# Kernel tuning notes

Hardware: AMD Instinct MI355X
Metric: run time of the kernel (lower is better)

Reference implementation:

```python
import jax, jax.numpy as jnp
import numpy as np

D = 256
H = 4
HD = D // H


def rotate_half(x):
    xp = x.reshape(x.shape[:-1] + (-1, 2))
    x1, x2 = xp[..., 0], xp[..., 1]
    return jnp.stack((-x2, x1), axis=-1).reshape(x.shape)


def apply_rope(freqs, t):
    # freqs: [2, B, 1, N, HD]; t: [B, H, N, HD]
    return t * freqs[0] + rotate_half(t) * freqs[1]


def layernorm(x, g, b, eps=1e-5):
    m = jnp.mean(x, axis=-1, keepdims=True)
    v = jnp.var(x, axis=-1, keepdims=True)
    return (x - m) * jax.lax.rsqrt(v + eps) * g + b


def ffn(z, W1, b1, g, be, W2, b2):
    h = layernorm(z @ W1 + b1, g, be)
    h = jax.nn.gelu(h, approximate=False)
    return h @ W2 + b2


def heads_split(t):
    B, N, _ = t.shape
    return t.reshape(B, N, H, HD).transpose(0, 2, 1, 3)  # [B,H,N,HD]


def heads_merge(t):
    B, h, N, hd = t.shape
    return t.transpose(0, 2, 1, 3).reshape(B, N, h * hd)


def sdpa(q, k, v):
    s = q.shape[-1] ** (-0.5)
    sim = jnp.einsum('bhid,bhjd->bhij', q, k) * s
    attn = jax.nn.softmax(sim, axis=-1)
    return jnp.einsum('bhij,bhjd->bhid', attn, v)


def self_block(x, enc, Wqkv, bqkv, Wo, bo, W1, b1, g, be, W2, b2):
    B, N, _ = x.shape
    qkv = (x @ Wqkv + bqkv).reshape(B, N, H, HD, 3).transpose(0, 2, 1, 3, 4)
    q, k, v = qkv[..., 0], qkv[..., 1], qkv[..., 2]
    q = apply_rope(enc, q)
    k = apply_rope(enc, k)
    msg = heads_merge(sdpa(q, k, v)) @ Wo + bo
    return x + ffn(jnp.concatenate([x, msg], axis=-1), W1, b1, g, be, W2, b2)


def cross_block(x0, x1, Wqk, bqk, Wv, bv, Wo, bo, W1, b1, g, be, W2, b2):
    qk0 = heads_split(x0 @ Wqk + bqk)
    qk1 = heads_split(x1 @ Wqk + bqk)
    v0 = heads_split(x0 @ Wv + bv)
    v1 = heads_split(x1 @ Wv + bv)
    s = HD ** (-0.5)
    qk0 = qk0 * (s ** 0.5)
    qk1 = qk1 * (s ** 0.5)
    sim = jnp.einsum('bhid,bhjd->bhij', qk0, qk1)
    attn01 = jax.nn.softmax(sim, axis=-1)
    attn10 = jax.nn.softmax(sim.transpose(0, 1, 3, 2), axis=-1)
    m0 = jnp.einsum('bhij,bhjd->bhid', attn01, v1)
    m1 = jnp.einsum('bhij,bhjd->bhid', attn10, v0)
    m0 = heads_merge(m0) @ Wo + bo
    m1 = heads_merge(m1) @ Wo + bo
    x0 = x0 + ffn(jnp.concatenate([x0, m0], axis=-1), W1, b1, g, be, W2, b2)
    x1 = x1 + ffn(jnp.concatenate([x1, m1], axis=-1), W1, b1, g, be, W2, b2)
    return x0, x1


def setup_inputs() -> dict:
    key = jax.random.key(0)
    ks = jax.random.split(key, 24)
    B, N = 4, 2048
    desc0 = jax.random.normal(ks[0], (B, N, D), jnp.float32)
    desc1 = jax.random.normal(ks[1], (B, N, D), jnp.float32)
    encoding0 = jax.random.uniform(ks[2], (2, B, 1, N, HD), jnp.float32)
    encoding1 = jax.random.uniform(ks[3], (2, B, 1, N, HD), jnp.float32)

    def lin(k, fin, fout):
        k1, k2 = jax.random.split(k)
        W = jax.random.normal(k1, (fin, fout), jnp.float32) * (fin ** -0.5)
        b = jax.random.normal(k2, (fout,), jnp.float32) * 0.01
        return W, b

    Wqkv, bqkv = lin(ks[4], D, 3 * D)
    Wo_s, bo_s = lin(ks[5], D, D)
    W1_s, b1_s = lin(ks[6], 2 * D, 2 * D)
    g_s = jnp.ones((2 * D,), jnp.float32)
    be_s = jnp.zeros((2 * D,), jnp.float32)
    W2_s, b2_s = lin(ks[7], 2 * D, D)
    Wqk_c, bqk_c = lin(ks[8], D, D)
    Wv_c, bv_c = lin(ks[9], D, D)
    Wo_c, bo_c = lin(ks[10], D, D)
    W1_c, b1_c = lin(ks[11], 2 * D, 2 * D)
    g_c = jnp.ones((2 * D,), jnp.float32)
    be_c = jnp.zeros((2 * D,), jnp.float32)
    W2_c, b2_c = lin(ks[12], 2 * D, D)
    return dict(desc0=desc0, desc1=desc1, encoding0=encoding0, encoding1=encoding1,
                Wqkv=Wqkv, bqkv=bqkv, Wo_s=Wo_s, bo_s=bo_s,
                W1_s=W1_s, b1_s=b1_s, g_s=g_s, be_s=be_s, W2_s=W2_s, b2_s=b2_s,
                Wqk_c=Wqk_c, bqk_c=bqk_c, Wv_c=Wv_c, bv_c=bv_c, Wo_c=Wo_c, bo_c=bo_c,
                W1_c=W1_c, b1_c=b1_c, g_c=g_c, be_c=be_c, W2_c=W2_c, b2_c=b2_c)


def reference(desc0, desc1, encoding0, encoding1,
              Wqkv, bqkv, Wo_s, bo_s, W1_s, b1_s, g_s, be_s, W2_s, b2_s,
              Wqk_c, bqk_c, Wv_c, bv_c, Wo_c, bo_c, W1_c, b1_c, g_c, be_c, W2_c, b2_c):
    d0 = self_block(desc0, encoding0, Wqkv, bqkv, Wo_s, bo_s, W1_s, b1_s, g_s, be_s, W2_s, b2_s)
    d1 = self_block(desc1, encoding1, Wqkv, bqkv, Wo_s, bo_s, W1_s, b1_s, g_s, be_s, W2_s, b2_s)
    return cross_block(d0, d1, Wqk_c, bqk_c, Wv_c, bv_c, Wo_c, bo_c, W1_c, b1_c, g_c, be_c, W2_c, b2_c)
```

## Files before the change

kernel.cpp:

```cpp
#include <hip/hip_runtime.h>
#include <math.h>

#define BB 4
#define HH 4
#define NN 2048
#define DD 256
#define HDIM 64
#define NTOK 8192
#define NTOK2 16384

typedef __attribute__((ext_vector_type(8))) __bf16 bf16x8;
typedef __attribute__((ext_vector_type(8))) unsigned short ushort8;
typedef __attribute__((ext_vector_type(4))) float floatx4;
typedef __attribute__((ext_vector_type(4))) short short4v;

union U8 { ushort8 u; bf16x8 b; };
union U4 { unsigned int u[2]; unsigned long long l; short4v s; };

#define MFMA16(a, b, c) __builtin_amdgcn_mfma_f32_16x16x16bf16_1k(a, b, c, 0, 0, 0)

__device__ __forceinline__ unsigned short f2bf(float x) {
    unsigned int u = __float_as_uint(x);
    u += 0x7FFF + ((u >> 16) & 1);
    return (unsigned short)(u >> 16);
}
__device__ __forceinline__ float bf2f(unsigned short u) {
    return __uint_as_float(((unsigned int)u) << 16);
}
__device__ __forceinline__ unsigned int cvtpk(float a, float b) {
    unsigned int r;
    asm("v_cvt_pk_bf16_f32 %0, %1, %2" : "=v"(r) : "v"(a), "v"(b));
    return r;
}
__device__ __forceinline__ floatx4 fmax4(floatx4 a, floatx4 b) {
    floatx4 r;
    r[0] = fmaxf(a[0], b[0]); r[1] = fmaxf(a[1], b[1]);
    r[2] = fmaxf(a[2], b[2]); r[3] = fmaxf(a[3], b[3]);
    return r;
}

struct WTab {
    const float* w[7];
    unsigned short* o[7];
    int K[7];
    int N[7];
    int st[7];
    int t0[8];
};

__global__ __launch_bounds__(256) void wtrans(WTab tab)
{
    __shared__ float lds[32][33];
    const int t = threadIdx.x;
    int bid = blockIdx.x;
    int s = 0;
    while (bid >= tab.t0[s + 1]) s++;
    const int ti = bid - tab.t0[s];
    const int K = tab.K[s], N = tab.N[s], st = tab.st[s];
    const int tx = ti % (N / 32), ty = ti / (N / 32);
    const int k0 = ty * 32, n0 = tx * 32;
    const float* W = tab.w[s];
    unsigned short* Wt = tab.o[s];

    {
        int r = t >> 3, c = (t & 7) * 4;
        float4 a = *(const float4*)&W[(size_t)(k0 + r) * N + n0 + c];
        lds[r][c] = a.x; lds[r][c+1] = a.y; lds[r][c+2] = a.z; lds[r][c+3] = a.w;
    }
    __syncthreads();
    {
        int n = t >> 3, kq = (t & 7) * 4;
        ushort4 p;
        p.x = f2bf(lds[kq+0][n]); p.y = f2bf(lds[kq+1][n]);
        p.z = f2bf(lds[kq+2][n]); p.w = f2bf(lds[kq+3][n]);
        *(ushort4*)&Wt[(size_t)(n0 + n) * st + k0 + kq] = p;
    }
}

__global__ __launch_bounds__(256) void wfuse(
    const float* __restrict__ Wo_s, const float* __restrict__ W1_s,
    unsigned short* __restrict__ o_s,
    const float* __restrict__ Wo_c, const float* __restrict__ W1_c,
    unsigned short* __restrict__ o_c)
{
    __shared__ float wo[32][33];
    __shared__ float w1[32][68];
    const int t = threadIdx.x;
    const int bid = blockIdx.x;
    const int seg = bid >> 6, ti_ = bid & 63;
    const int i0 = (ti_ >> 3) * 32, n0 = (ti_ & 7) * 64;
    const float* Wo  = seg ? Wo_c : Wo_s;
    const float* W1b = (seg ? W1_c : W1_s) + 256 * 512;
    unsigned short* out = seg ? o_c : o_s;
    const int ti = t >> 3, tn = t & 7;

    float acc[8] = {};
    for (int jc = 0; jc < 256; jc += 32) {
        {
            int r = t >> 3, c = (t & 7) * 4;
            *(float4*)&wo[r][c] = *(const float4*)&Wo[(size_t)(i0 + r) * 256 + jc + c];
            int c8 = (t & 7) * 8;
            *(float4*)&w1[r][c8]     = *(const float4*)&W1b[(size_t)(jc + r) * 512 + n0 + c8];
            *(float4*)&w1[r][c8 + 4] = *(const float4*)&W1b[(size_t)(jc + r) * 512 + n0 + c8 + 4];
        }
        __syncthreads();
        #pragma unroll
        for (int j = 0; j < 32; j++) {
            float a = wo[ti][j];
            #pragma unroll
            for (int e = 0; e < 8; e++) acc[e] += a * w1[j][tn * 8 + e];
        }
        __syncthreads();
    }
    #pragma unroll
    for (int e = 0; e < 8; e++)
        out[(size_t)(n0 + tn * 8 + e) * 512 + 256 + i0 + ti] = f2bf(acc[e]);
}

__global__ __launch_bounds__(256) void bfuse(
    const float* bo_s, const float* W1_s, const float* b1_s, float* bs,
    const float* bo_c, const float* W1_c, const float* b1_c, float* bc)
{
    __shared__ float r[4];
    const int bid = blockIdx.x;
    const int seg = bid >> 9, n = bid & 511;
    const float* bo  = seg ? bo_c : bo_s;
    const float* W1b = (seg ? W1_c : W1_s) + 256 * 512;
    const float* b1  = seg ? b1_c : b1_s;
    float* out       = seg ? bc : bs;
    const int j = threadIdx.x;
    float a = bo[j] * W1b[(size_t)j * 512 + n];
    #pragma unroll
    for (int o = 32; o > 0; o >>= 1) a += __shfl_xor(a, o, 64);
    if ((j & 63) == 0) r[j >> 6] = a;
    __syncthreads();
    if (j == 0) out[n] = b1[n] + r[0] + r[1] + r[2] + r[3];
}

__global__ __launch_bounds__(256) void gemm_mfma(
    const unsigned short* __restrict__ A, int lda,
    const unsigned short* __restrict__ Wt, int K,
    const float* __restrict__ bias, const float* __restrict__ bias2, int mode,
    float* outF, unsigned short* outH0, unsigned short* outH1,
    unsigned short* outH2,
    int ldc, const float* R0, const float* R1)
{
    __shared__ __align__(16) unsigned short As[64 * 72];
    __shared__ __align__(16) unsigned short Bs[128 * 72];
    const int t = threadIdx.x;
    const int w = t >> 6, lane = t & 63, quad = lane >> 4, l15 = lane & 15;
    const int m0 = blockIdx.y * 64, n0 = blockIdx.x * 128;
    const int wn = w * 32;
    const int sar = t >> 2, sac = (t & 3) * 16;
    const int sbr = t >> 1, sbc = (t & 1) * 32;

    const unsigned short* Ap = A  + (size_t)(m0 + sar) * lda + sac;
    const unsigned short* Bp = Wt + (size_t)(n0 + sbr) * K   + sbc;

    ushort8 pa0 = *(const ushort8*)(Ap);
    ushort8 pa1 = *(const ushort8*)(Ap + 8);
    ushort8 pb0 = *(const ushort8*)(Bp);
    ushort8 pb1 = *(const ushort8*)(Bp + 8);
    ushort8 pb2 = *(const ushort8*)(Bp + 16);
    ushort8 pb3 = *(const ushort8*)(Bp + 24);

    floatx4 acc[4][2];
    #pragma unroll
    for (int i = 0; i < 4; i++)
        #pragma unroll
        for (int j = 0; j < 2; j++) acc[i][j] = (floatx4){0.f, 0.f, 0.f, 0.f};

    const int nk = K >> 6;
    for (int kk = 0; kk < nk; kk++) {
        *(ushort8*)&As[sar * 72 + sac]      = pa0;
        *(ushort8*)&As[sar * 72 + sac + 8]  = pa1;
        *(ushort8*)&Bs[sbr * 72 + sbc]      = pb0;
        *(ushort8*)&Bs[sbr * 72 + sbc + 8]  = pb1;
        *(ushort8*)&Bs[sbr * 72 + sbc + 16] = pb2;
        *(ushort8*)&Bs[sbr * 72 + sbc + 24] = pb3;
        __syncthreads();
        if (kk + 1 < nk) {
            int ko = (kk + 1) * 64;
            pa0 = *(const ushort8*)(Ap + ko);
            pa1 = *(const ushort8*)(Ap + ko + 8);
            pb0 = *(const ushort8*)(Bp + ko);
            pb1 = *(const ushort8*)(Bp + ko + 8);
            pb2 = *(const ushort8*)(Bp + ko + 16);
            pb3 = *(const ushort8*)(Bp + ko + 24);
        }
        #pragma unroll
        for (int kh = 0; kh < 2; kh++) {
            U8 af[4], bf[2];
            #pragma unroll
            for (int i = 0; i < 4; i++)
                af[i].u = *(const ushort8*)&As[(i * 16 + l15) * 72 + kh * 32 + quad * 8];
            #pragma unroll
            for (int j = 0; j < 2; j++)
                bf[j].u = *(const ushort8*)&Bs[(wn + j * 16 + l15) * 72 + kh * 32 + quad * 8];
            #pragma unroll
            for (int i = 0; i < 4; i++)
                #pragma unroll
                for (int j = 0; j < 2; j++)
                    acc[i][j] = __builtin_amdgcn_mfma_f32_16x16x32_bf16(af[i].b, bf[j].b, acc[i][j], 0, 0, 0);
        }
        __syncthreads();
    }

    #pragma unroll
    for (int i = 0; i < 4; i++) {
        #pragma unroll
        for (int j = 0; j < 2; j++) {
            int col = n0 + wn + j * 16 + l15;
            float bv = (mode == 2 && col >= 256) ? bias2[col & 255] : bias[col];
            #pragma unroll
            for (int r = 0; r < 4; r++) {
                int grow = m0 + i * 16 + quad * 4 + r;
                float v = acc[i][j][r] + bv;
                if (mode == 1) {
                    outH0[(size_t)grow * ldc + col] = f2bf(v);
                } else if (mode == 2) {
                    int cc = col & 255;
                    int h = cc >> 6, d = cc & 63;
                    int ds = grow >> 13, b = (grow >> 11) & 3, n = grow & 2047;
                    int bh = ds * 16 + b * 4 + h;
                    if (col < 256)
                        outH0[((size_t)bh * NN + n) * HDIM + d] = f2bf(v);
                    else
                        outH1[((size_t)bh * HDIM + d) * NN + n] = f2bf(v);
                } else if (mode == 3) {
                    int sel = col % 3, cc = col / 3;
                    int h = cc >> 6, d = cc & 63;
                    int ds = grow >> 13, b = (grow >> 11) & 3, n = grow & 2047;
                    int bh = ds * 16 + b * 4 + h;
                    if (sel == 0)
                        outH0[((size_t)bh * NN + n) * HDIM + d] = f2bf(v);
                    else if (sel == 1)
                        outH1[((size_t)bh * NN + n) * HDIM + d] = f2bf(v);
                    else
                        outH2[((size_t)bh * HDIM + d) * NN + n] = f2bf(v);
                } else {
                    const float* R = (grow < NTOK) ? R0 : R1;
                    float vv = v + R[(size_t)(grow & 8191) * 256 + col];
                    outF[(size_t)grow * 256 + col] = vv;
                    if (outH0) outH0[(size_t)grow * 256 + col] = f2bf(vv);
                    if (outH1) outH1[(size_t)grow * 512 + col] = f2bf(vv);
                }
            }
        }
    }
}

__global__ __launch_bounds__(256) void rope_k(unsigned short* __restrict__ qb,
                                              unsigned short* __restrict__ kb,
                                              const float* __restrict__ enc0,
                                              const float* __restrict__ enc1)
{
    int i = blockIdx.x * 256 + threadIdx.x;
    int dp = (i & 31) * 2;
    int n  = (i >> 5) & (NN - 1);
    int h  = (i >> 16) & 3;
    int b  = (i >> 18) & 3;
    int ds = (i >> 20) & 1;
    int bf = (i >> 21) & 1;
    unsigned short* tq = (bf ? kb : qb) +
        (((size_t)(ds * 16 + b * 4 + h)) * NN + n) * HDIM + dp;
    const float* e0 = (ds ? enc1 : enc0) + ((size_t)b * NN + n) * HDIM + dp;
    const float* e1 = e0 + (size_t)BB * NN * HDIM;
    float x0 = bf2f(tq[0]), x1 = bf2f(tq[1]);
    float y0 = x0 * e0[0] - x1 * e1[0];
    float y1 = x1 * e0[1] + x0 * e1[1];
    tq[0] = f2bf(y0); tq[1] = f2bf(y1);
}

__global__ __launch_bounds__(256) void flash_attn(
    const unsigned short* __restrict__ Q, const unsigned short* __restrict__ K,
    const unsigned short* __restrict__ V, unsigned short* __restrict__ O,
    int ldo, int kvx, float qscale)
{
    __shared__ __align__(16) unsigned short Ks[2][64 * 72];
    __shared__ __align__(16) unsigned short Vt[2][64 * 72];

    const int t    = threadIdx.x;
    const int w    = t >> 6;
    const int lane = t & 63;
    const int quad = lane >> 4;
    const int l15  = lane & 15;
    const int bh   = blockIdx.y;
    const int kbh  = bh ^ kvx;
    const int q0   = blockIdx.x * 64;

    const unsigned short* Qb  = Q + (size_t)bh  * NN * HDIM;
    const unsigned short* Kb  = K + (size_t)kbh * NN * HDIM;
    const unsigned short* VTb = V + (size_t)kbh * NN * HDIM;

    const int srf = t >> 3, scf = (t & 7) * 8;

    bf16x8 qf0, qf1;
    {
        const int qrow = q0 + w * 16 + l15;
        U8 r0, r1, x0, x1;
        r0.u = *(const ushort8*)&Qb[(size_t)qrow * HDIM + quad * 8];
        r1.u = *(const ushort8*)&Qb[(size_t)qrow * HDIM + 32 + quad * 8];
        #pragma unroll
        for (int j = 0; j < 8; j++) {
            x0.u[j] = f2bf(bf2f(r0.u[j]) * qscale);
            x1.u[j] = f2bf(bf2f(r1.u[j]) * qscale);
        }
        qf0 = x0.b; qf1 = x1.b;
    }

    floatx4 o[4];
    #pragma unroll
    for (int c = 0; c < 4; c++) o[c] = (floatx4){0.f, 0.f, 0.f, 0.f};
    float m = -1e30f, l = 0.f;

    ushort8 ka0 = *(const ushort8*)&Kb[(size_t)srf * HDIM + scf];
    ushort8 ka1 = *(const ushort8*)&Kb[(size_t)(srf + 32) * HDIM + scf];
    ushort8 va0 = *(const ushort8*)&VTb[(size_t)srf * NN + scf];
    ushort8 va1 = *(const ushort8*)&VTb[(size_t)(srf + 32) * NN + scf];
    *(ushort8*)&Ks[0][srf * 72 + scf]        = ka0;
    *(ushort8*)&Ks[0][(srf + 32) * 72 + scf] = ka1;
    *(ushort8*)&Vt[0][srf * 72 + scf]        = va0;
    *(ushort8*)&Vt[0][(srf + 32) * 72 + scf] = va1;
    __syncthreads();

    int cur = 0;
    for (int j0 = 0; j0 < NN; j0 += 64, cur ^= 1) {
        const int more = (j0 + 64 < NN);
        if (more) {
            const int jn = j0 + 64;
            ka0 = *(const ushort8*)&Kb[(size_t)(jn + srf) * HDIM + scf];
            ka1 = *(const ushort8*)&Kb[(size_t)(jn + srf + 32) * HDIM + scf];
            va0 = *(const ushort8*)&VTb[(size_t)srf * NN + jn + scf];
            va1 = *(const ushort8*)&VTb[(size_t)(srf + 32) * NN + jn + scf];
        }

        floatx4 s[4];
        __builtin_amdgcn_s_setprio(1);
        #pragma unroll
        for (int t4 = 0; t4 < 4; t4++) {
            U8 k0, k1;
            k0.u = *(const ushort8*)&Ks[cur][(t4 * 16 + l15) * 72 + quad * 8];
            k1.u = *(const ushort8*)&Ks[cur][(t4 * 16 + l15) * 72 + 32 + quad * 8];
            floatx4 z = (floatx4){0.f, 0.f, 0.f, 0.f};
            z = __builtin_amdgcn_mfma_f32_16x16x32_bf16(k0.b, qf0, z, 0, 0, 0);
            z = __builtin_amdgcn_mfma_f32_16x16x32_bf16(k1.b, qf1, z, 0, 0, 0);
            s[t4] = z;
        }
        __builtin_amdgcn_s_setprio(0);

        floatx4 a = fmax4(fmax4(s[0], s[1]), fmax4(s[2], s[3]));
        float mx = fmaxf(fmaxf(a[0], a[1]), fmaxf(a[2], a[3]));
        mx = fmaxf(mx, __shfl_xor(mx, 16, 64));
        mx = fmaxf(mx, __shfl_xor(mx, 32, 64));
        if (!__all(mx <= m + 8.f)) {
            float mn = fmaxf(m, mx);
            float al = exp2f(m - mn);
            m = mn;
            l *= al;
            #pragma unroll
            for (int c = 0; c < 4; c++)
                #pragma unroll
                for (int r = 0; r < 4; r++) o[c][r] *= al;
        }
        float rs = 0.f;
        #pragma unroll
        for (int t4 = 0; t4 < 4; t4++)
            #pragma unroll
            for (int r = 0; r < 4; r++) {
                float p = exp2f(s[t4][r] - m);
                s[t4][r] = p;
                rs += p;
            }
        l += rs;

        short4v pf[4];
        #pragma unroll
        for (int t4 = 0; t4 < 4; t4++) {
            U4 pk;
            pk.u[0] = cvtpk(s[t4][0], s[t4][1]);
            pk.u[1] = cvtpk(s[t4][2], s[t4][3]);
            pf[t4] = pk.s;
        }

        __builtin_amdgcn_s_setprio(1);
        #pragma unroll
        for (int c = 0; c < 4; c++) {
            U4 vf[4];
            #pragma unroll
            for (int t4 = 0; t4 < 4; t4++)
                vf[t4].l = *(const unsigned long long*)
                    &Vt[cur][(c * 16 + l15) * 72 + t4 * 16 + quad * 4];
            #pragma unroll
            for (int t4 = 0; t4 < 4; t4++)
                o[c] = MFMA16(vf[t4].s, pf[t4], o[c]);
        }
        __builtin_amdgcn_s_setprio(0);

        if (more) {
            *(ushort8*)&Ks[cur ^ 1][srf * 72 + scf]        = ka0;
            *(ushort8*)&Ks[cur ^ 1][(srf + 32) * 72 + scf] = ka1;
            *(ushort8*)&Vt[cur ^ 1][srf * 72 + scf]        = va0;
            *(ushort8*)&Vt[cur ^ 1][(srf + 32) * 72 + scf] = va1;
            __syncthreads();
        }
    }

    l += __shfl_xor(l, 16, 64);
    l += __shfl_xor(l, 32, 64);
    const int ds = bh >> 4, b = (bh >> 2) & 3, h = bh & 3;
    const int q = q0 + w * 16 + l15;
    const size_t row = (size_t)ds * NTOK + b * NN + q;
    float inv = 1.f / l;
    #pragma unroll
    for (int c = 0; c < 4; c++) {
        U4 pk;
        pk.u[0] = cvtpk(o[c][0] * inv, o[c][1] * inv);
        pk.u[1] = cvtpk(o[c][2] * inv, o[c][3] * inv);
        *(unsigned long long*)&O[row * ldo + h * HDIM + c * 16 + quad * 4] = pk.l;
    }
}

__global__ __launch_bounds__(256) void ln_gelu(
    unsigned short* __restrict__ hb, const float* __restrict__ g,
    const float* __restrict__ be)
{
    const int lane = threadIdx.x & 63;
    const int wv   = threadIdx.x >> 6;
    const size_t row = (size_t)blockIdx.x * 4 + wv;
    unsigned short* ip = hb + row * 512 + lane * 8;
    U8 v; v.u = *(const ushort8*)ip;
    float x[8];
    float s = 0.f, ss = 0.f;
    #pragma unroll
    for (int j = 0; j < 8; j++) {
        x[j] = bf2f(v.u[j]);
        s += x[j];
        ss += x[j] * x[j];
    }
    #pragma unroll
    for (int o = 32; o > 0; o >>= 1) {
        s  += __shfl_xor(s, o, 64);
        ss += __shfl_xor(ss, o, 64);
    }
    float mean = s * (1.f / 512.f);
    float var  = ss * (1.f / 512.f) - mean * mean;
    float inv  = rsqrtf(var + 1e-5f);
    float4 g0 = *(const float4*)&g[lane * 8];
    float4 g1 = *(const float4*)&g[lane * 8 + 4];
    float4 b0 = *(const float4*)&be[lane * 8];
    float4 b1 = *(const float4*)&be[lane * 8 + 4];
    float gg[8] = {g0.x, g0.y, g0.z, g0.w, g1.x, g1.y, g1.z, g1.w};
    float bb[8] = {b0.x, b0.y, b0.z, b0.w, b1.x, b1.y, b1.z, b1.w};
    #pragma unroll
    for (int j = 0; j < 8; j++) {
        float y = (x[j] - mean) * inv * gg[j] + bb[j];
        v.u[j] = f2bf(0.5f * y * (1.f + erff(y * 0.70710678f)));
    }
    *(ushort8*)ip = v.u;
}

__global__ __launch_bounds__(256) void copy_to_cat(
    const float* __restrict__ s0, const float* __restrict__ s1,
    unsigned short* __restrict__ cat)
{
    int i = blockIdx.x * 256 + threadIdx.x;
    int row = i >> 6, c4 = (i & 63) * 4;
    const float* s = (row < NTOK) ? s0 : s1;
    float4 a = *(const float4*)&s[(size_t)(row & 8191) * 256 + c4];
    ushort4 p = { f2bf(a.x), f2bf(a.y), f2bf(a.z), f2bf(a.w) };
    *(ushort4*)&cat[(size_t)row * 512 + c4] = p;
}

extern "C" void kernel_launch(void* const* d_in, const int* in_sizes, int n_in,
                              void* d_out, int out_size, void* d_ws, size_t ws_size,
                              hipStream_t stream)
{
    const float* desc0 = (const float*)d_in[0];
    const float* desc1 = (const float*)d_in[1];
    const float* enc0  = (const float*)d_in[2];
    const float* enc1  = (const float*)d_in[3];
    const float* Wqkv  = (const float*)d_in[4];  const float* bqkv  = (const float*)d_in[5];
    const float* Wo_s  = (const float*)d_in[6];  const float* bo_s  = (const float*)d_in[7];
    const float* W1_s  = (const float*)d_in[8];  const float* b1_s  = (const float*)d_in[9];
    const float* g_s   = (const float*)d_in[10]; const float* be_s  = (const float*)d_in[11];
    const float* W2_s  = (const float*)d_in[12]; const float* b2_s  = (const float*)d_in[13];
    const float* Wqk_c = (const float*)d_in[14]; const float* bqk_c = (const float*)d_in[15];
    const float* Wv_c  = (const float*)d_in[16]; const float* bv_c  = (const float*)d_in[17];
    const float* Wo_c  = (const float*)d_in[18]; const float* bo_c  = (const float*)d_in[19];
    const float* W1_c  = (const float*)d_in[20]; const float* b1_c  = (const float*)d_in[21];
    const float* g_c   = (const float*)d_in[22]; const float* be_c  = (const float*)d_in[23];
    const float* W2_c  = (const float*)d_in[24]; const float* b2_c  = (const float*)d_in[25];

    char* ws = (char*)d_ws;
    unsigned short* wt  = (unsigned short*)ws;
    unsigned short* qb  = (unsigned short*)(ws + 2490368);
    unsigned short* kb  = (unsigned short*)(ws + 10878976);
    unsigned short* vb  = (unsigned short*)(ws + 27656192);
    unsigned short* cat = (unsigned short*)(ws + 36044800);
    unsigned short* hb  = (unsigned short*)(ws + 52822016);
    unsigned short* dbf = (unsigned short*)(ws + 86376448);

    unsigned short* t_qkv  = wt;
    float*          bias_s = (float*)(wt + 196608);
    unsigned short* t_w1s  = wt + 262144;
    unsigned short* t_w2s  = wt + 524288;
    unsigned short* t_wqkc = wt + 655360;
    float*          bias_c = (float*)(wt + 786432);
    unsigned short* t_w1c  = wt + 851968;
    unsigned short* t_w2c  = wt + 1114112;

    float* outF = (float*)d_out;

    dim3 blk(256);

    WTab tab;
    tab.w[0] = Wqkv;  tab.o[0] = t_qkv;          tab.K[0] = 256; tab.N[0] = 768; tab.st[0] = 256;
    tab.w[1] = W1_s;  tab.o[1] = t_w1s;          tab.K[1] = 256; tab.N[1] = 512; tab.st[1] = 512;
    tab.w[2] = W2_s;  tab.o[2] = t_w2s;          tab.K[2] = 512; tab.N[2] = 256; tab.st[2] = 512;
    tab.w[3] = Wqk_c; tab.o[3] = t_wqkc;         tab.K[3] = 256; tab.N[3] = 256; tab.st[3] = 256;
    tab.w[4] = Wv_c;  tab.o[4] = t_wqkc + 65536; tab.K[4] = 256; tab.N[4] = 256; tab.st[4] = 256;
    tab.w[5] = W1_c;  tab.o[5] = t_w1c;          tab.K[5] = 256; tab.N[5] = 512; tab.st[5] = 512;
    tab.w[6] = W2_c;  tab.o[6] = t_w2c;          tab.K[6] = 512; tab.N[6] = 256; tab.st[6] = 512;
    int acc_t = 0;
    for (int s = 0; s < 7; s++) {
        tab.t0[s] = acc_t;
        acc_t += (tab.K[s] / 32) * (tab.N[s] / 32);
    }
    tab.t0[7] = acc_t;
    hipLaunchKernelGGL(wtrans, dim3(acc_t), blk, 0, stream, tab);
    hipLaunchKernelGGL(wfuse, dim3(128), blk, 0, stream,
                       Wo_s, W1_s, t_w1s, Wo_c, W1_c, t_w1c);
    hipLaunchKernelGGL(bfuse, dim3(1024), blk, 0, stream,
                       bo_s, W1_s, b1_s, bias_s, bo_c, W1_c, b1_c, bias_c);

    auto gemm = [&](const unsigned short* A, int lda, const unsigned short* Wtp,
                    int K, const float* bias, const float* bias2, int Nc, int mode,
                    float* oF, unsigned short* oh0, unsigned short* oh1,
                    unsigned short* oh2, int ldc, const float* r0, const float* r1) {
        dim3 g(Nc / 128, NTOK2 / 64);
        hipLaunchKernelGGL(gemm_mfma, g, blk, 0, stream,
                           A, lda, Wtp, K, bias, bias2, mode,
                           oF, oh0, oh1, oh2, ldc, r0, r1);
    };

    const float QS = 0.125f * 1.44269504088896f;

    hipLaunchKernelGGL(copy_to_cat, dim3(4096), blk, 0, stream, desc0, desc1, cat);
    gemm(cat, 512, t_qkv, 256, bqkv, nullptr, 768, 3,
         nullptr, qb, kb, vb, 0, nullptr, nullptr);
    hipLaunchKernelGGL(rope_k, dim3(16384), blk, 0, stream, qb, kb, enc0, enc1);
    hipLaunchKernelGGL(flash_attn, dim3(NN / 64, 32), blk, 0, stream,
                       qb, kb, vb, cat + 256, 512, 0, QS);
    gemm(cat, 512, t_w1s, 512, bias_s, nullptr, 512, 1,
         nullptr, hb, nullptr, nullptr, 512, nullptr, nullptr);
    hipLaunchKernelGGL(ln_gelu, dim3(NTOK2 / 4), blk, 0, stream, hb, g_s, be_s);
    gemm(hb, 512, t_w2s, 512, b2_s, nullptr, 256, 4,
         outF, dbf, cat, nullptr, 256, desc0, desc1);

    gemm(dbf, 256, t_wqkc, 256, bqk_c, bv_c, 512, 2,
         nullptr, qb, vb, nullptr, 0, nullptr, nullptr);
    hipLaunchKernelGGL(flash_attn, dim3(NN / 64, 32), blk, 0, stream,
                       qb, qb, vb, cat + 256, 512, 16, QS);
    gemm(cat, 512, t_w1c, 512, bias_c, nullptr, 512, 1,
         nullptr, hb, nullptr, nullptr, 512, nullptr, nullptr);
    hipLaunchKernelGGL(ln_gelu, dim3(NTOK2 / 4), blk, 0, stream, hb, g_c, be_c);
    gemm(hb, 512, t_w2c, 512, b2_c, nullptr, 256, 4,
         outF, nullptr, nullptr, nullptr, 256, outF, outF + (size_t)NTOK * 256);
}
```

Measured before the change: 459.0 us.

## Load GEMM MFMA fragments directly from global memory, dropping LDS staging

The tiled GEMM no longer stages A and W tiles through shared memory with register prefetch and barriers. Each wave now loads its MFMA operand fragments straight from global memory every 32-wide K step. This removes LDS writes, reads and __syncthreads, but gives up the sharing of A fragments across the four waves. Each wave now re-fetches the same A rows, and the software prefetch that overlapped loads with MFMAs is lost, so the kernel depends on L1/L2 hits and load latency.

```diff
diff --git a/kernel.cpp b/kernel.cpp
--- a/kernel.cpp
+++ b/kernel.cpp
@@ -145,24 +145,15 @@
     unsigned short* outH2,
     int ldc, const float* R0, const float* R1)
 {
-    __shared__ __align__(16) unsigned short As[64 * 72];
-    __shared__ __align__(16) unsigned short Bs[128 * 72];
     const int t = threadIdx.x;
     const int w = t >> 6, lane = t & 63, quad = lane >> 4, l15 = lane & 15;
     const int m0 = blockIdx.y * 64, n0 = blockIdx.x * 128;
     const int wn = w * 32;
-    const int sar = t >> 2, sac = (t & 3) * 16;
-    const int sbr = t >> 1, sbc = (t & 1) * 32;
-
-    const unsigned short* Ap = A  + (size_t)(m0 + sar) * lda + sac;
-    const unsigned short* Bp = Wt + (size_t)(n0 + sbr) * K   + sbc;
-
-    ushort8 pa0 = *(const ushort8*)(Ap);
-    ushort8 pa1 = *(const ushort8*)(Ap + 8);
-    ushort8 pb0 = *(const ushort8*)(Bp);
-    ushort8 pb1 = *(const ushort8*)(Bp + 8);
-    ushort8 pb2 = *(const ushort8*)(Bp + 16);
-    ushort8 pb3 = *(const ushort8*)(Bp + 24);
+
+    const unsigned short* Ar = A  + (size_t)(m0 + l15) * lda      + quad * 8;
+    const unsigned short* Br = Wt + (size_t)(n0 + wn + l15) * K   + quad * 8;
+    const size_t a16 = (size_t)16 * lda;
+    const size_t b16 = (size_t)16 * K;
 
     floatx4 acc[4][2];
     #pragma unroll
@@ -170,40 +161,21 @@
         #pragma unroll
         for (int j = 0; j < 2; j++) acc[i][j] = (floatx4){0.f, 0.f, 0.f, 0.f};
 
-    const int nk = K >> 6;
+    const int nk = K >> 5;
     for (int kk = 0; kk < nk; kk++) {
-        *(ushort8*)&As[sar * 72 + sac]      = pa0;
-        *(ushort8*)&As[sar * 72 + sac + 8]  = pa1;
-        *(ushort8*)&Bs[sbr * 72 + sbc]      = pb0;
-        *(ushort8*)&Bs[sbr * 72 + sbc + 8]  = pb1;
-        *(ushort8*)&Bs[sbr * 72 + sbc + 16] = pb2;
-        *(ushort8*)&Bs[sbr * 72 + sbc + 24] = pb3;
-        __syncthreads();
-        if (kk + 1 < nk) {
-            int ko = (kk + 1) * 64;
-            pa0 = *(const ushort8*)(Ap + ko);
-            pa1 = *(const ushort8*)(Ap + ko + 8);
-            pb0 = *(const ushort8*)(Bp + ko);
-            pb1 = *(const ushort8*)(Bp + ko + 8);
-            pb2 = *(const ushort8*)(Bp + ko + 16);
-            pb3 = *(const ushort8*)(Bp + ko + 24);
-        }
-        #pragma unroll
-        for (int kh = 0; kh < 2; kh++) {
-            U8 af[4], bf[2];
-            #pragma unroll
-            for (int i = 0; i < 4; i++)
-                af[i].u = *(const ushort8*)&As[(i * 16 + l15) * 72 + kh * 32 + quad * 8];
+        const int ko = kk * 32;
+        U8 af[4], bf[2];
+        #pragma unroll
+        for (int i = 0; i < 4; i++)
+            af[i].u = *(const ushort8*)(Ar + (size_t)i * a16 + ko);
+        #pragma unroll
+        for (int j = 0; j < 2; j++)
+            bf[j].u = *(const ushort8*)(Br + (size_t)j * b16 + ko);
+        #pragma unroll
+        for (int i = 0; i < 4; i++)
             #pragma unroll
             for (int j = 0; j < 2; j++)
-                bf[j].u = *(const ushort8*)&Bs[(wn + j * 16 + l15) * 72 + kh * 32 + quad * 8];
-            #pragma unroll
-            for (int i = 0; i < 4; i++)
-                #pragma unroll
-                for (int j = 0; j < 2; j++)
-                    acc[i][j] = __builtin_amdgcn_mfma_f32_16x16x32_bf16(af[i].b, bf[j].b, acc[i][j], 0, 0, 0);
-        }
-        __syncthreads();
+                acc[i][j] = __builtin_amdgcn_mfma_f32_16x16x32_bf16(af[i].b, bf[j].b, acc[i][j], 0, 0, 0);
     }
 
     #pragma unroll
```

After: 578.3 us. 26.0% more time.
